# Kernel optimization log

Hardware: AMD Instinct MI355X
Metric: run time of the kernel (lower is better)

The kernel has to match this reference:

```python
import jax, jax.numpy as jnp
import numpy as np

N = 20_000_000
B = 16_384


def setup_inputs() -> dict:
    key = jax.random.key(0)
    k1, k2, k3 = jax.random.split(key, 3)
    inp = jax.random.normal(k1, (N,), dtype=jnp.float32)
    tgt = jax.random.normal(k2, (N,), dtype=jnp.float32)
    batch = jnp.sort(jax.random.randint(k3, (N,), 0, B, dtype=jnp.int64))
    return {"input": inp, "target": tgt, "batch": batch, "batch_size": B}


def reference(input, target, batch, batch_size):
    # sum_j c_ij @ c_ij.T over a segment == (segment_sum c)^2
    seg_in = jax.ops.segment_sum(input, batch, num_segments=batch_size)
    seg_tg = jax.ops.segment_sum(target, batch, num_segments=batch_size)
    dot_in = seg_in * seg_in          # [B]
    dot_tg = seg_tg * seg_tg          # [B]
    loss_dot = jnp.sum((dot_in - dot_tg) ** 2)            # F.mse_loss(..., 'sum')
    loss_elem = jnp.sum((jnp.abs(input) - jnp.abs(target)) ** 2)
    return loss_dot + loss_elem
```

## Files before the change

kernel.cpp:

```cpp
#include <hip/hip_runtime.h>

#define BSEG  16384
#define NPART 256
#define WS_BYTES (2 * BSEG * 4 + NPART * 8)

__global__ __launch_bounds__(256) void main_pass(
        const float* __restrict__ in, const float* __restrict__ tg,
        const int* __restrict__ batch,
        float* __restrict__ seg_in, float* __restrict__ seg_tg,
        double* __restrict__ elem_part, int n)
{
    const int tid  = blockIdx.x * blockDim.x + threadIdx.x;
    const int lane = threadIdx.x & 63;
    const long long i0 = (long long)tid * 8;

    float elem = 0.0f;
    int   cur  = -1;
    float si = 0.0f, st = 0.0f;

    if (i0 < n) {
        const float4* in4 = reinterpret_cast<const float4*>(in + i0);
        const float4* tg4 = reinterpret_cast<const float4*>(tg + i0);
        const int4*   b4  = reinterpret_cast<const int4*>(batch + i0);

        float4 a0 = in4[0], a1 = in4[1];
        float4 t0 = tg4[0], t1 = tg4[1];
        int4   c0 = b4[0],  c1 = b4[1];

        float vi[8] = {a0.x, a0.y, a0.z, a0.w, a1.x, a1.y, a1.z, a1.w};
        float vt[8] = {t0.x, t0.y, t0.z, t0.w, t1.x, t1.y, t1.z, t1.w};
        int   vb[8] = {c0.x, c0.y, c0.z, c0.w, c1.x, c1.y, c1.z, c1.w};

        cur = vb[0];
        #pragma unroll
        for (int j = 0; j < 8; ++j) {
            float x = vi[j], y = vt[j];
            float d = fabsf(x) - fabsf(y);
            elem = fmaf(d, d, elem);
            int b = vb[j];
            if (b != cur) {
                atomicAdd(seg_in + cur, si);
                atomicAdd(seg_tg + cur, st);
                cur = b; si = 0.0f; st = 0.0f;
            }
            si += x; st += y;
        }
    }

    int prevId = __shfl_up(cur, 1);
    int f = (lane == 0) || (prevId != cur);
    #pragma unroll
    for (int d = 1; d < 64; d <<= 1) {
        float o1 = __shfl_up(si, d);
        float o2 = __shfl_up(st, d);
        int   of = __shfl_up(f,  d);
        if (lane >= d) {
            if (!f) { si += o1; st += o2; }
            f |= of;
        }
    }
    int nextId = __shfl_down(cur, 1);
    bool isTail = (lane == 63) || (nextId != cur);
    if (isTail && cur >= 0) {
        atomicAdd(seg_in + cur, si);
        atomicAdd(seg_tg + cur, st);
    }

    #pragma unroll
    for (int off = 32; off; off >>= 1) elem += __shfl_xor(elem, off);
    __shared__ float wsum[4];
    int wid = threadIdx.x >> 6;
    if (lane == 0) wsum[wid] = elem;
    __syncthreads();
    if (threadIdx.x == 0) {
        float s = wsum[0] + wsum[1] + wsum[2] + wsum[3];
        atomicAdd(elem_part + (blockIdx.x & (NPART - 1)), (double)s);
    }
}

__global__ __launch_bounds__(1024) void finalize_kernel(
        const float* __restrict__ seg_in, const float* __restrict__ seg_tg,
        const double* __restrict__ elem_part, float* __restrict__ out)
{
    double acc = 0.0;
    for (int i = threadIdx.x; i < BSEG; i += 1024) {
        float a = seg_in[i], b = seg_tg[i];
        float d = a * a - b * b;
        acc += (double)d * (double)d;
    }
    if (threadIdx.x < NPART) acc += elem_part[threadIdx.x];
    #pragma unroll
    for (int off = 32; off; off >>= 1) acc += __shfl_xor(acc, off);
    __shared__ double wsum[16];
    int lane = threadIdx.x & 63, wid = threadIdx.x >> 6;
    if (lane == 0) wsum[wid] = acc;
    __syncthreads();
    if (threadIdx.x == 0) {
        double t = 0.0;
        #pragma unroll
        for (int w = 0; w < 16; ++w) t += wsum[w];
        out[0] = (float)t;
    }
}

extern "C" void kernel_launch(void* const* d_in, const int* in_sizes, int n_in,
                              void* d_out, int out_size, void* d_ws, size_t ws_size,
                              hipStream_t stream) {
    const float* in    = (const float*)d_in[0];
    const float* tg    = (const float*)d_in[1];
    const int*   batch = (const int*)d_in[2];
    const int n = in_sizes[0];

    float*  seg_in    = (float*)d_ws;
    float*  seg_tg    = seg_in + BSEG;
    double* elem_part = (double*)(seg_in + 2 * BSEG);
    float*  out       = (float*)d_out;

    hipMemsetAsync(d_ws, 0, WS_BYTES, stream);

    const int nthreads = n / 8;
    const int blocks   = (nthreads + 255) / 256;
    main_pass<<<blocks, 256, 0, stream>>>(in, tg, batch, seg_in, seg_tg, elem_part, n);

    finalize_kernel<<<1, 1024, 0, stream>>>(seg_in, seg_tg, elem_part, out);
}
```

Measured before the change: 232.4 us.

## Process multiple tiles per wave with carried segment sums and prefetch

Each wavefront now walks TILE=8 consecutive 512-element chunks instead of one. It carries the running sum of the last segment across chunks so fewer atomics are issued per segment, and it software-prefetches the next chunk's loads. The launch grid shrinks by a factor of eight. The finalize kernel is vectorized with float4 loads. The trade-off is fewer waves in flight and more complex carry logic with possible correctness edge cases.

```diff
diff --git a/kernel.cpp b/kernel.cpp
--- a/kernel.cpp
+++ b/kernel.cpp
@@ -2,6 +2,8 @@
 
 #define BSEG  16384
 #define NPART 256
+#define TILE  8
+#define WAVE_SPAN (512LL * TILE)
 #define WS_BYTES (2 * BSEG * 4 + NPART * 8)
 
 __global__ __launch_bounds__(256) void main_pass(
@@ -10,60 +12,99 @@
         float* __restrict__ seg_in, float* __restrict__ seg_tg,
         double* __restrict__ elem_part, int n)
 {
-    const int tid  = blockIdx.x * blockDim.x + threadIdx.x;
     const int lane = threadIdx.x & 63;
-    const long long i0 = (long long)tid * 8;
+    const int gw   = (blockIdx.x * blockDim.x + threadIdx.x) >> 6;
+    const long long waveBase = (long long)gw * WAVE_SPAN;
 
     float elem = 0.0f;
-    int   cur  = -1;
-    float si = 0.0f, st = 0.0f;
+    int   carryId = -1;
+    float carrySi = 0.0f, carrySt = 0.0f;
 
-    if (i0 < n) {
-        const float4* in4 = reinterpret_cast<const float4*>(in + i0);
-        const float4* tg4 = reinterpret_cast<const float4*>(tg + i0);
-        const int4*   b4  = reinterpret_cast<const int4*>(batch + i0);
-
-        float4 a0 = in4[0], a1 = in4[1];
-        float4 t0 = tg4[0], t1 = tg4[1];
-        int4   c0 = b4[0],  c1 = b4[1];
-
-        float vi[8] = {a0.x, a0.y, a0.z, a0.w, a1.x, a1.y, a1.z, a1.w};
-        float vt[8] = {t0.x, t0.y, t0.z, t0.w, t1.x, t1.y, t1.z, t1.w};
-        int   vb[8] = {c0.x, c0.y, c0.z, c0.w, c1.x, c1.y, c1.z, c1.w};
-
-        cur = vb[0];
-        #pragma unroll
-        for (int j = 0; j < 8; ++j) {
-            float x = vi[j], y = vt[j];
-            float d = fabsf(x) - fabsf(y);
-            elem = fmaf(d, d, elem);
-            int b = vb[j];
-            if (b != cur) {
-                atomicAdd(seg_in + cur, si);
-                atomicAdd(seg_tg + cur, st);
-                cur = b; si = 0.0f; st = 0.0f;
-            }
-            si += x; st += y;
+    float4 a0, a1, t0, t1; int4 b0, b1;
+    {
+        long long i0 = waveBase + (long long)lane * 8;
+        if (i0 < n) {
+            a0 = ((const float4*)(in + i0))[0];  a1 = ((const float4*)(in + i0))[1];
+            t0 = ((const float4*)(tg + i0))[0];  t1 = ((const float4*)(tg + i0))[1];
+            b0 = ((const int4*)(batch + i0))[0]; b1 = ((const int4*)(batch + i0))[1];
         }
     }
 
-    int prevId = __shfl_up(cur, 1);
-    int f = (lane == 0) || (prevId != cur);
     #pragma unroll
-    for (int d = 1; d < 64; d <<= 1) {
-        float o1 = __shfl_up(si, d);
-        float o2 = __shfl_up(st, d);
-        int   of = __shfl_up(f,  d);
-        if (lane >= d) {
-            if (!f) { si += o1; st += o2; }
-            f |= of;
+    for (int t = 0; t < TILE; ++t) {
+        const long long i0 = waveBase + (long long)t * 512 + (long long)lane * 8;
+        const bool live = (i0 < n);
+
+        float4 na0, na1, nt0, nt1; int4 nb0, nb1;
+        if (t + 1 < TILE) {
+            long long ni0 = waveBase + (long long)(t + 1) * 512 + (long long)lane * 8;
+            if (ni0 < n) {
+                na0 = ((const float4*)(in + ni0))[0];  na1 = ((const float4*)(in + ni0))[1];
+                nt0 = ((const float4*)(tg + ni0))[0];  nt1 = ((const float4*)(tg + ni0))[1];
+                nb0 = ((const int4*)(batch + ni0))[0]; nb1 = ((const int4*)(batch + ni0))[1];
+            }
         }
+
+        int   cur = -2;
+        float si = 0.0f, st = 0.0f;
+        if (live) {
+            float vi[8] = {a0.x, a0.y, a0.z, a0.w, a1.x, a1.y, a1.z, a1.w};
+            float vt[8] = {t0.x, t0.y, t0.z, t0.w, t1.x, t1.y, t1.z, t1.w};
+            int   vb[8] = {b0.x, b0.y, b0.z, b0.w, b1.x, b1.y, b1.z, b1.w};
+            cur = vb[0];
+            #pragma unroll
+            for (int j = 0; j < 8; ++j) {
+                float x = vi[j], y = vt[j];
+                float d = fabsf(x) - fabsf(y);
+                elem = fmaf(d, d, elem);
+                int b = vb[j];
+                if (b != cur) {
+                    atomicAdd(seg_in + cur, si);
+                    atomicAdd(seg_tg + cur, st);
+                    cur = b; si = 0.0f; st = 0.0f;
+                }
+                si += x; st += y;
+            }
+        }
+
+        #pragma unroll
+        for (int d = 1; d < 64; d <<= 1) {
+            float o1 = __shfl_up(si, d);
+            float o2 = __shfl_up(st, d);
+            int  oid = __shfl_up(cur, d);
+            if (lane >= d && oid == cur) { si += o1; st += o2; }
+        }
+        const int   firstId = __shfl(cur, 0);
+        const int   lastId  = __shfl(cur, 63);
+        const float lastSi  = __shfl(si, 63);
+        const float lastSt  = __shfl(st, 63);
+        const int   nextId  = __shfl_down(cur, 1);
+        const bool  isTail  = (lane == 63) || (nextId != cur);
+
+        if (lane == 0 && carryId >= 0 && carryId != firstId) {
+            atomicAdd(seg_in + carryId, carrySi);
+            atomicAdd(seg_tg + carryId, carrySt);
+        }
+        if (isTail && cur >= 0 && cur != lastId) {
+            float fi = si, ft = st;
+            if (cur == firstId && carryId == firstId) { fi += carrySi; ft += carrySt; }
+            atomicAdd(seg_in + cur, fi);
+            atomicAdd(seg_tg + cur, ft);
+        }
+        if (lastId >= 0) {
+            if (carryId == lastId && firstId == lastId) { carrySi += lastSi; carrySt += lastSt; }
+            else                                        { carrySi  = lastSi; carrySt  = lastSt; }
+            carryId = lastId;
+        } else {
+            carryId = -1; carrySi = 0.0f; carrySt = 0.0f;
+        }
+
+        if (t + 1 < TILE) { a0 = na0; a1 = na1; t0 = nt0; t1 = nt1; b0 = nb0; b1 = nb1; }
     }
-    int nextId = __shfl_down(cur, 1);
-    bool isTail = (lane == 63) || (nextId != cur);
-    if (isTail && cur >= 0) {
-        atomicAdd(seg_in + cur, si);
-        atomicAdd(seg_tg + cur, st);
+
+    if (lane == 0 && carryId >= 0) {
+        atomicAdd(seg_in + carryId, carrySi);
+        atomicAdd(seg_tg + carryId, carrySt);
     }
 
     #pragma unroll
@@ -82,11 +123,16 @@
         const float* __restrict__ seg_in, const float* __restrict__ seg_tg,
         const double* __restrict__ elem_part, float* __restrict__ out)
 {
+    const float4* s4 = (const float4*)seg_in;
+    const float4* g4 = (const float4*)seg_tg;
     double acc = 0.0;
-    for (int i = threadIdx.x; i < BSEG; i += 1024) {
-        float a = seg_in[i], b = seg_tg[i];
-        float d = a * a - b * b;
-        acc += (double)d * (double)d;
+    for (int i = threadIdx.x; i < BSEG / 4; i += 1024) {
+        float4 a = s4[i], b = g4[i];
+        float d0 = a.x * a.x - b.x * b.x;
+        float d1 = a.y * a.y - b.y * b.y;
+        float d2 = a.z * a.z - b.z * b.z;
+        float d3 = a.w * a.w - b.w * b.w;
+        acc += (double)d0 * d0 + (double)d1 * d1 + (double)d2 * d2 + (double)d3 * d3;
     }
     if (threadIdx.x < NPART) acc += elem_part[threadIdx.x];
     #pragma unroll
@@ -118,8 +164,8 @@
 
     hipMemsetAsync(d_ws, 0, WS_BYTES, stream);
 
-    const int nthreads = n / 8;
-    const int blocks   = (nthreads + 255) / 256;
+    const int nWaves = (int)((n + WAVE_SPAN - 1) / WAVE_SPAN);
+    const int blocks = (nWaves + 3) / 4;
     main_pass<<<blocks, 256, 0, stream>>>(in, tg, batch, seg_in, seg_tg, elem_part, n);
 
     finalize_kernel<<<1, 1024, 0, stream>>>(seg_in, seg_tg, elem_part, out);
```

Result: slower. 239.8 us (+3.2%).

## Replicate segment accumulators per block group and parallelize final segment reduction

Applied to the files above, without the earlier changes.

Segment partial sums now go to up to 64 replicated accumulator arrays, chosen by block index, to reduce atomic contention on shared addresses. The single-block finalize is split into a multi-block reduction over the replicas plus a small combine kernel. The elem partial slots are padded to separate cache lines, and the segmented warp scan now compares segment ids directly instead of carrying flags. In exchange it adds a larger workspace memset, extra replica reads, and one more kernel launch.

```diff
diff --git a/kernel.cpp b/kernel.cpp
--- a/kernel.cpp
+++ b/kernel.cpp
@@ -1,19 +1,25 @@
 #include <hip/hip_runtime.h>
 
-#define BSEG  16384
-#define NPART 256
-#define WS_BYTES (2 * BSEG * 4 + NPART * 8)
+#define BSEG   16384
+#define NPART  256
+#define RMAX   64
 
-__global__ __launch_bounds__(256) void main_pass(
+static inline size_t ws_need(int R) {
+    return (size_t)R * 2 * BSEG * 4 + (size_t)NPART * 8 * 8 + 8;
+}
+
+__global__ __launch_bounds__(256, 4) void main_pass(
         const float* __restrict__ in, const float* __restrict__ tg,
         const int* __restrict__ batch,
-        float* __restrict__ seg_in, float* __restrict__ seg_tg,
-        double* __restrict__ elem_part, int n)
+        float* __restrict__ rep, double* __restrict__ elem_part,
+        int n, int rmask)
 {
     const int tid  = blockIdx.x * blockDim.x + threadIdx.x;
     const int lane = threadIdx.x & 63;
+    float* seg_in = rep + (size_t)(blockIdx.x & rmask) * (2 * BSEG);
+    float* seg_tg = seg_in + BSEG;
+
     const long long i0 = (long long)tid * 8;
-
     float elem = 0.0f;
     int   cur  = -1;
     float si = 0.0f, st = 0.0f;
@@ -47,20 +53,15 @@
         }
     }
 
-    int prevId = __shfl_up(cur, 1);
-    int f = (lane == 0) || (prevId != cur);
     #pragma unroll
     for (int d = 1; d < 64; d <<= 1) {
         float o1 = __shfl_up(si, d);
         float o2 = __shfl_up(st, d);
-        int   of = __shfl_up(f,  d);
-        if (lane >= d) {
-            if (!f) { si += o1; st += o2; }
-            f |= of;
-        }
+        int  oid = __shfl_up(cur, d);
+        if (lane >= d && oid == cur) { si += o1; st += o2; }
     }
-    int nextId = __shfl_down(cur, 1);
-    bool isTail = (lane == 63) || (nextId != cur);
+    const int  nextId = __shfl_down(cur, 1);
+    const bool isTail = (lane == 63) || (nextId != cur);
     if (isTail && cur >= 0) {
         atomicAdd(seg_in + cur, si);
         atomicAdd(seg_tg + cur, st);
@@ -74,33 +75,44 @@
     __syncthreads();
     if (threadIdx.x == 0) {
         float s = wsum[0] + wsum[1] + wsum[2] + wsum[3];
-        atomicAdd(elem_part + (blockIdx.x & (NPART - 1)), (double)s);
+        atomicAdd(elem_part + (size_t)(blockIdx.x & (NPART - 1)) * 8, (double)s);
     }
 }
 
-__global__ __launch_bounds__(1024) void finalize_kernel(
-        const float* __restrict__ seg_in, const float* __restrict__ seg_tg,
-        const double* __restrict__ elem_part, float* __restrict__ out)
+__global__ __launch_bounds__(256) void seg_reduce(
+        const float* __restrict__ rep, int R, double* __restrict__ acc)
 {
-    double acc = 0.0;
-    for (int i = threadIdx.x; i < BSEG; i += 1024) {
-        float a = seg_in[i], b = seg_tg[i];
-        float d = a * a - b * b;
-        acc += (double)d * (double)d;
+    const int s = blockIdx.x * 256 + threadIdx.x;
+    float si = 0.0f, st = 0.0f;
+    for (int r = 0; r < R; ++r) {
+        si += rep[(size_t)r * 2 * BSEG + s];
+        st += rep[(size_t)r * 2 * BSEG + BSEG + s];
     }
-    if (threadIdx.x < NPART) acc += elem_part[threadIdx.x];
+    float d = si * si - st * st;
+    double a = (double)d * (double)d;
     #pragma unroll
-    for (int off = 32; off; off >>= 1) acc += __shfl_xor(acc, off);
-    __shared__ double wsum[16];
+    for (int off = 32; off; off >>= 1) a += __shfl_xor(a, off);
+    __shared__ double wsum[4];
     int lane = threadIdx.x & 63, wid = threadIdx.x >> 6;
-    if (lane == 0) wsum[wid] = acc;
+    if (lane == 0) wsum[wid] = a;
     __syncthreads();
-    if (threadIdx.x == 0) {
-        double t = 0.0;
-        #pragma unroll
-        for (int w = 0; w < 16; ++w) t += wsum[w];
-        out[0] = (float)t;
-    }
+    if (threadIdx.x == 0)
+        atomicAdd(acc, wsum[0] + wsum[1] + wsum[2] + wsum[3]);
+}
+
+__global__ __launch_bounds__(256) void final_combine(
+        const double* __restrict__ elem_part, const double* __restrict__ acc,
+        float* __restrict__ out)
+{
+    double v = elem_part[(size_t)threadIdx.x * 8];
+    #pragma unroll
+    for (int off = 32; off; off >>= 1) v += __shfl_xor(v, off);
+    __shared__ double wsum[4];
+    int lane = threadIdx.x & 63, wid = threadIdx.x >> 6;
+    if (lane == 0) wsum[wid] = v;
+    __syncthreads();
+    if (threadIdx.x == 0)
+        out[0] = (float)(wsum[0] + wsum[1] + wsum[2] + wsum[3] + *acc);
 }
 
 extern "C" void kernel_launch(void* const* d_in, const int* in_sizes, int n_in,
@@ -111,16 +123,20 @@
     const int*   batch = (const int*)d_in[2];
     const int n = in_sizes[0];
 
-    float*  seg_in    = (float*)d_ws;
-    float*  seg_tg    = seg_in + BSEG;
-    double* elem_part = (double*)(seg_in + 2 * BSEG);
+    int R = 1;
+    while (R < RMAX && ws_need(R * 2) <= ws_size) R *= 2;
+
+    float*  rep       = (float*)d_ws;
+    double* elem_part = (double*)(rep + (size_t)R * 2 * BSEG);
+    double* acc       = elem_part + (size_t)NPART * 8;
     float*  out       = (float*)d_out;
 
-    hipMemsetAsync(d_ws, 0, WS_BYTES, stream);
+    hipMemsetAsync(d_ws, 0, ws_need(R), stream);
 
     const int nthreads = n / 8;
     const int blocks   = (nthreads + 255) / 256;
-    main_pass<<<blocks, 256, 0, stream>>>(in, tg, batch, seg_in, seg_tg, elem_part, n);
+    main_pass<<<blocks, 256, 0, stream>>>(in, tg, batch, rep, elem_part, n, R - 1);
 
-    finalize_kernel<<<1, 1024, 0, stream>>>(seg_in, seg_tg, elem_part, out);
+    seg_reduce<<<BSEG / 256, 256, 0, stream>>>(rep, R, acc);
+    final_combine<<<1, 256, 0, stream>>>(elem_part, acc, out);
 }
```

Result: slower. 251.8 us (+8.4%).
